# Optimization experiments

Measured on AMD Instinct MI355X. Metric: run time of the kernel, lower is better.

## Reference

```python
import jax, jax.numpy as jnp
import numpy as np

N = 50000        # nodes
E = 800000       # directed edges (before self-loops)
F_IN = 128       # num_features
GAT_DIM = 16     # per-head channels
HEADS = 4
HID = GAT_DIM * HEADS   # 64, concat output of each GATConv
FC = 10 * GAT_DIM       # 160
OUT = 64                # output_dim
NEG_SLOPE = 0.2         # PyG GATConv default


def _gat_conv(x, W, a_src, a_dst, b, src, dst):
    """One PyG-style GATConv (concat=True, self-loops already in src/dst).
    x: [N, Fin], W: [Fin, HEADS*GAT_DIM], a_src/a_dst: [HEADS, GAT_DIM], b: [HEADS*GAT_DIM]."""
    H, C = a_src.shape
    h = (x @ W).reshape(N, H, C)                       # [N,H,C]
    s_src = (h * a_src).sum(-1)                        # [N,H] per-node src score
    s_dst = (h * a_dst).sum(-1)                        # [N,H]
    e = jax.nn.leaky_relu(s_src[src] + s_dst[dst], NEG_SLOPE)  # [Etot,H]
    # segment softmax over incoming edges of each destination node
    m = jax.ops.segment_max(e, dst, num_segments=N)    # [N,H]
    ex = jnp.exp(e - m[dst])
    z = jax.ops.segment_sum(ex, dst, num_segments=N)   # [N,H]
    alpha = ex / (z[dst] + 1e-16)                      # [Etot,H]
    msg = h[src] * alpha[:, :, None]                   # [Etot,H,C]
    out = jax.ops.segment_sum(msg, dst, num_segments=N)
    return out.reshape(N, H * C) + b


def setup_inputs() -> dict:
    key = jax.random.key(0)
    ks = jax.random.split(key, 20)
    sc = 0.05
    inp = {
        "x": jax.random.normal(ks[0], (N, F_IN), dtype=jnp.float32),
        "edge_index": jax.random.randint(ks[1], (2, E), 0, N, dtype=jnp.int32),
        "W0": jax.random.normal(ks[2], (F_IN, HID), dtype=jnp.float32) * sc,
        "as0": jax.random.normal(ks[3], (HEADS, GAT_DIM), dtype=jnp.float32) * sc,
        "ad0": jax.random.normal(ks[4], (HEADS, GAT_DIM), dtype=jnp.float32) * sc,
        "b0": jnp.zeros((HID,), jnp.float32),
        "W1": jax.random.normal(ks[5], (HID, HID), dtype=jnp.float32) * sc,
        "as1": jax.random.normal(ks[6], (HEADS, GAT_DIM), dtype=jnp.float32) * sc,
        "ad1": jax.random.normal(ks[7], (HEADS, GAT_DIM), dtype=jnp.float32) * sc,
        "b1": jnp.zeros((HID,), jnp.float32),
        "W2": jax.random.normal(ks[8], (HID, HID), dtype=jnp.float32) * sc,
        "as2": jax.random.normal(ks[9], (HEADS, GAT_DIM), dtype=jnp.float32) * sc,
        "ad2": jax.random.normal(ks[10], (HEADS, GAT_DIM), dtype=jnp.float32) * sc,
        "b2": jnp.zeros((HID,), jnp.float32),
        "fw1": jax.random.normal(ks[11], (HID, FC), dtype=jnp.float32) * sc,
        "fb1": jnp.zeros((FC,), jnp.float32),
        "fw2": jax.random.normal(ks[12], (FC, OUT), dtype=jnp.float32) * sc,
        "fb2": jnp.zeros((OUT,), jnp.float32),
    }
    return inp


def reference(x, edge_index, W0, as0, ad0, b0, W1, as1, ad1, b1, W2, as2, ad2, b2, fw1, fb1, fw2, fb2):
    loop = jnp.arange(N, dtype=edge_index.dtype)
    src = jnp.concatenate([edge_index[0], loop])   # PyG add_self_loops=True
    dst = jnp.concatenate([edge_index[1], loop])
    h = jax.nn.relu(_gat_conv(x, W0, as0, ad0, b0, src, dst))
    h = jax.nn.relu(_gat_conv(h, W1, as1, ad1, b1, src, dst))
    h = jax.nn.relu(_gat_conv(h, W2, as2, ad2, b2, src, dst))
    h = jax.nn.relu(h @ fw1 + fb1)
    return h @ fw2 + fb2
```

## Files before the change

### kernel.cpp

```cpp
#include <hip/hip_runtime.h>
#include <hip/hip_fp16.h>

#define NN 50000
#define EE 800000
#define ETOT (EE + NN)
#define HIDD 64
#define NHEADS 4
#define FCD 160
#define OUTD 64

#define NBKT 196
#define BSTRIDE 5120
#define CHUNK 4096
#define NEBLK ((ETOT + CHUNK - 1) / CHUNK)
#define NGB   ((NN + 63) / 64)
#define NFC128 ((NN + 127) / 128)


__global__ void k_zero(int* __restrict__ cursor) {
    int t = threadIdx.x;
    if (t < NBKT) cursor[t] = 0;
}

__global__ __launch_bounds__(256) void k_binwrite(const int* __restrict__ ei,
                                                  int* __restrict__ cursor,
                                                  unsigned* __restrict__ binned) {
    __shared__ int hist[NBKT];
    __shared__ int sbase[NBKT];
    __shared__ int cur[NBKT];
    int t = threadIdx.x;
    for (int i = t; i < NBKT; i += 256) hist[i] = 0;
    __syncthreads();
    int base = blockIdx.x * CHUNK;
    for (int k = t; k < CHUNK; k += 256) {
        int i = base + k;
        if (i < ETOT) {
            int dst = (i < EE) ? ei[EE + i] : (i - EE);
            atomicAdd(&hist[dst >> 8], 1);
        }
    }
    __syncthreads();
    for (int b = t; b < NBKT; b += 256) {
        int c = hist[b];
        sbase[b] = b * BSTRIDE + (c ? atomicAdd(&cursor[b], c) : 0);
        cur[b] = 0;
    }
    __syncthreads();
    for (int k = t; k < CHUNK; k += 256) {
        int i = base + k;
        if (i < ETOT) {
            int src, dst;
            if (i < EE) { src = ei[i]; dst = ei[EE + i]; }
            else { src = dst = i - EE; }
            int b = dst >> 8;
            int p = atomicAdd(&cur[b], 1);
            binned[sbase[b] + p] = ((unsigned)src << 8) | (unsigned)(dst & 255);
        }
    }
}

__global__ __launch_bounds__(256) void k_csr_final(const int* __restrict__ cursor,
                                                   const unsigned* __restrict__ binned,
                                                   int* __restrict__ rowbeg,
                                                   int* __restrict__ rowend,
                                                   int* __restrict__ csrc) {
    __shared__ int hist[256];
    __shared__ int cur[256];
    __shared__ int wsum[4];
    int b = blockIdx.x;
    int t = threadIdx.x;
    int s0 = b * BSTRIDE;
    int cnt = cursor[b];
    hist[t] = 0;
    __syncthreads();
    for (int k = t; k < cnt; k += 256) {
        unsigned pr = binned[s0 + k];
        atomicAdd(&hist[pr & 255u], 1);
    }
    __syncthreads();
    int v = hist[t];
    int lane = t & 63, w = t >> 6;
    int x = v;
    #pragma unroll
    for (int off = 1; off < 64; off <<= 1) {
        int y = __shfl_up(x, off);
        if (lane >= off) x += y;
    }
    if (lane == 63) wsum[w] = x;
    __syncthreads();
    int add = 0;
    #pragma unroll
    for (int k = 0; k < 4; k++) add += (k < w) ? wsum[k] : 0;
    int excl = x + add - v;
    int n = (b << 8) + t;
    if (n < NN) {
        rowbeg[n] = s0 + excl;
        rowend[n] = s0 + excl + v;
    }
    cur[t] = s0 + excl;
    __syncthreads();
    for (int k = t; k < cnt; k += 256) {
        unsigned pr = binned[s0 + k];
        int p = atomicAdd(&cur[pr & 255u], 1);
        csrc[p] = (int)(pr >> 8);
    }
}


template<int FIN>
__global__ __launch_bounds__(256) void k_gemm_scores(
        const float* __restrict__ x, const float* __restrict__ W,
        const float* __restrict__ a_src, const float* __restrict__ a_dst,
        __half* __restrict__ h, float* __restrict__ ssrc, float* __restrict__ sdst) {
    __shared__ float wl[64 * 64];
    __shared__ float xt[64][68];
    int t = threadIdx.x;
    int nb = blockIdx.x * 64;
    int qg = t & 15, ng = t >> 4;
    float acc[4][4] = {};
    const float4* wl4 = (const float4*)wl;

    #pragma unroll
    for (int p = 0; p < FIN / 64; p++) {
        if (p) __syncthreads();
        for (int i = t; i < 64 * 64 / 4; i += 256)
            ((float4*)wl)[i] = ((const float4*)W)[p * 1024 + i];
        #pragma unroll
        for (int r = 0; r < 4; r++) {
            int idx = t + r * 256;
            int node = idx & 63, kq = idx >> 6;
            int n = nb + node;
            float4 v = make_float4(0.f, 0.f, 0.f, 0.f);
            if (n < NN) v = *(const float4*)(x + (size_t)n * FIN + p * 64 + kq * 4);
            xt[kq * 4 + 0][node] = v.x;
            xt[kq * 4 + 1][node] = v.y;
            xt[kq * 4 + 2][node] = v.z;
            xt[kq * 4 + 3][node] = v.w;
        }
        __syncthreads();
        #pragma unroll 4
        for (int k = 0; k < 64; k++) {
            float4 wv = wl4[k * 16 + qg];
            float4 xv = *(const float4*)&xt[k][ng * 4];
            acc[0][0] += xv.x * wv.x; acc[0][1] += xv.x * wv.y;
            acc[0][2] += xv.x * wv.z; acc[0][3] += xv.x * wv.w;
            acc[1][0] += xv.y * wv.x; acc[1][1] += xv.y * wv.y;
            acc[1][2] += xv.y * wv.z; acc[1][3] += xv.y * wv.w;
            acc[2][0] += xv.z * wv.x; acc[2][1] += xv.z * wv.y;
            acc[2][2] += xv.z * wv.z; acc[2][3] += xv.z * wv.w;
            acc[3][0] += xv.w * wv.x; acc[3][1] += xv.w * wv.y;
            acc[3][2] += xv.w * wv.z; acc[3][3] += xv.w * wv.w;
        }
    }

    #pragma unroll
    for (int r = 0; r < 4; r++) {
        int n = nb + ng * 4 + r;
        if (n < NN) {
            union { __half2 h2[2]; uint2 u; } pk;
            pk.h2[0] = __floats2half2_rn(acc[r][0], acc[r][1]);
            pk.h2[1] = __floats2half2_rn(acc[r][2], acc[r][3]);
            *(uint2*)(h + (size_t)n * HIDD + qg * 4) = pk.u;
        }
    }

    float as0 = a_src[qg * 4 + 0], as1 = a_src[qg * 4 + 1];
    float as2 = a_src[qg * 4 + 2], as3 = a_src[qg * 4 + 3];
    float ad0 = a_dst[qg * 4 + 0], ad1 = a_dst[qg * 4 + 1];
    float ad2 = a_dst[qg * 4 + 2], ad3 = a_dst[qg * 4 + 3];
    float vs[4], vd[4];
    #pragma unroll
    for (int r = 0; r < 4; r++) {
        vs[r] = acc[r][0] * as0 + acc[r][1] * as1 + acc[r][2] * as2 + acc[r][3] * as3;
        vd[r] = acc[r][0] * ad0 + acc[r][1] * ad1 + acc[r][2] * ad2 + acc[r][3] * ad3;
        vs[r] += __shfl_xor(vs[r], 1); vs[r] += __shfl_xor(vs[r], 2);
        vd[r] += __shfl_xor(vd[r], 1); vd[r] += __shfl_xor(vd[r], 2);
    }
    if ((qg & 3) == 0) {
        int hd = qg >> 2;
        #pragma unroll
        for (int r = 0; r < 4; r++) {
            int n = nb + ng * 4 + r;
            if (n < NN) {
                ssrc[n * NHEADS + hd] = vs[r];
                sdst[n * NHEADS + hd] = vd[r];
            }
        }
    }
}


__global__ __launch_bounds__(256) void k_aggr(
        const __half* __restrict__ h, const float* __restrict__ ssrc,
        const float* __restrict__ sdst, const int* __restrict__ rowbeg,
        const int* __restrict__ rowend,
        const int* __restrict__ csrc, const float* __restrict__ bias,
        float* __restrict__ out) {
    int wid  = threadIdx.x >> 6;
    int lane = threadIdx.x & 63;
    int n = blockIdx.x * 4 + wid;
    int sub = lane >> 4;
    int c4  = lane & 15;
    int hd  = c4 >> 2;
    int beg = rowbeg[n], end = rowend[n];
    float sdh = sdst[n * NHEADS + hd];

    float4 acc = make_float4(0.f, 0.f, 0.f, 0.f);
    float z = 0.f;
    for (int cb = beg; cb < end; cb += 16) {
        #pragma unroll
        for (int o = 0; o < 4; o++) {
            int e = cb + sub + o * 4;
            if (e < end) {
                int s = csrc[e];
                float eh = ssrc[s * NHEADS + hd] + sdh;
                eh = eh > 0.f ? eh : 0.2f * eh;
                float w = __expf(eh);
                uint2 r = *(const uint2*)(h + (size_t)s * HIDD + c4 * 4);
                float2 lo = __half22float2(*(__half2*)&r.x);
                float2 hi = __half22float2(*(__half2*)&r.y);
                acc.x += lo.x * w; acc.y += lo.y * w;
                acc.z += hi.x * w; acc.w += hi.y * w;
                z += w;
            }
        }
    }
    acc.x += __shfl_xor(acc.x, 16); acc.y += __shfl_xor(acc.y, 16);
    acc.z += __shfl_xor(acc.z, 16); acc.w += __shfl_xor(acc.w, 16);
    z += __shfl_xor(z, 16);
    acc.x += __shfl_xor(acc.x, 32); acc.y += __shfl_xor(acc.y, 32);
    acc.z += __shfl_xor(acc.z, 32); acc.w += __shfl_xor(acc.w, 32);
    z += __shfl_xor(z, 32);

    if (sub == 0) {
        float inv_z = 1.0f / (z + 1e-16f);
        float4 bv = *(const float4*)(bias + c4 * 4);
        float4 o;
        o.x = acc.x * inv_z + bv.x; o.x = o.x > 0.f ? o.x : 0.f;
        o.y = acc.y * inv_z + bv.y; o.y = o.y > 0.f ? o.y : 0.f;
        o.z = acc.z * inv_z + bv.z; o.z = o.z > 0.f ? o.z : 0.f;
        o.w = acc.w * inv_z + bv.w; o.w = o.w > 0.f ? o.w : 0.f;
        *(float4*)(out + (size_t)n * HIDD + c4 * 4) = o;
    }
}


__global__ __launch_bounds__(256) void k_fc_fused(const float* __restrict__ x,
        const float* __restrict__ W1, const float* __restrict__ b1,
        const float* __restrict__ W2, const float* __restrict__ b2,
        float* __restrict__ out) {
    __shared__ float wl[32 * 160];
    __shared__ float xt[32][132];
    __shared__ __half y[160][136];
    int t = threadIdx.x;
    int nb = blockIdx.x * 128;
    const float4* wl4 = (const float4*)wl;

    {
        int qg = t & 7, ng = t >> 3;
        float acc[4][5][4] = {};
        #pragma unroll
        for (int p = 0; p < 2; p++) {
            if (p) __syncthreads();
            for (int i = t; i < 32 * 160 / 4; i += 256)
                ((float4*)wl)[i] = ((const float4*)W1)[p * 32 * 40 + i];
            #pragma unroll
            for (int r = 0; r < 4; r++) {
                int idx = t + r * 256;
                int node = idx & 127, kq = idx >> 7;
                int n = nb + node;
                float4 v = make_float4(0.f, 0.f, 0.f, 0.f);
                if (n < NN) v = *(const float4*)(x + (size_t)n * 64 + p * 32 + kq * 4);
                xt[kq * 4 + 0][node] = v.x;
                xt[kq * 4 + 1][node] = v.y;
                xt[kq * 4 + 2][node] = v.z;
                xt[kq * 4 + 3][node] = v.w;
            }
            __syncthreads();
            #pragma unroll 4
            for (int k = 0; k < 32; k++) {
                float4 xv = *(const float4*)&xt[k][ng * 4];
                #pragma unroll
                for (int i = 0; i < 5; i++) {
                    float4 wv = wl4[k * 40 + qg + 8 * i];
                    acc[0][i][0] += xv.x * wv.x; acc[0][i][1] += xv.x * wv.y;
                    acc[0][i][2] += xv.x * wv.z; acc[0][i][3] += xv.x * wv.w;
                    acc[1][i][0] += xv.y * wv.x; acc[1][i][1] += xv.y * wv.y;
                    acc[1][i][2] += xv.y * wv.z; acc[1][i][3] += xv.y * wv.w;
                    acc[2][i][0] += xv.z * wv.x; acc[2][i][1] += xv.z * wv.y;
                    acc[2][i][2] += xv.z * wv.z; acc[2][i][3] += xv.z * wv.w;
                    acc[3][i][0] += xv.w * wv.x; acc[3][i][1] += xv.w * wv.y;
                    acc[3][i][2] += xv.w * wv.z; acc[3][i][3] += xv.w * wv.w;
                }
            }
        }
        #pragma unroll
        for (int i = 0; i < 5; i++) {
            int j0 = (qg + 8 * i) * 4;
            float4 bv = *(const float4*)(b1 + j0);
            #pragma unroll
            for (int r = 0; r < 4; r++) {
                int node = ng * 4 + r;
                float v0 = acc[r][i][0] + bv.x; v0 = v0 > 0.f ? v0 : 0.f;
                float v1 = acc[r][i][1] + bv.y; v1 = v1 > 0.f ? v1 : 0.f;
                float v2 = acc[r][i][2] + bv.z; v2 = v2 > 0.f ? v2 : 0.f;
                float v3 = acc[r][i][3] + bv.w; v3 = v3 > 0.f ? v3 : 0.f;
                y[j0 + 0][node] = __float2half_rn(v0);
                y[j0 + 1][node] = __float2half_rn(v1);
                y[j0 + 2][node] = __float2half_rn(v2);
                y[j0 + 3][node] = __float2half_rn(v3);
            }
        }
    }
    __syncthreads();

    {
        int qg = t & 15, ng = t >> 4;
        float acc[8][4] = {};
        #pragma unroll
        for (int p = 0; p < 2; p++) {
            if (p) __syncthreads();
            for (int i = t; i < 80 * 64 / 4; i += 256)
                ((float4*)wl)[i] = ((const float4*)W2)[p * 80 * 16 + i];
            __syncthreads();
            #pragma unroll 2
            for (int k = 0; k < 80; k++) {
                float4 wv = wl4[k * 16 + qg];
                uint4 yr = *(const uint4*)&y[p * 80 + k][ng * 8];
                float2 f0 = __half22float2(*(__half2*)&yr.x);
                float2 f1 = __half22float2(*(__half2*)&yr.y);
                float2 f2 = __half22float2(*(__half2*)&yr.z);
                float2 f3 = __half22float2(*(__half2*)&yr.w);
                acc[0][0] += f0.x * wv.x; acc[0][1] += f0.x * wv.y;
                acc[0][2] += f0.x * wv.z; acc[0][3] += f0.x * wv.w;
                acc[1][0] += f0.y * wv.x; acc[1][1] += f0.y * wv.y;
                acc[1][2] += f0.y * wv.z; acc[1][3] += f0.y * wv.w;
                acc[2][0] += f1.x * wv.x; acc[2][1] += f1.x * wv.y;
                acc[2][2] += f1.x * wv.z; acc[2][3] += f1.x * wv.w;
                acc[3][0] += f1.y * wv.x; acc[3][1] += f1.y * wv.y;
                acc[3][2] += f1.y * wv.z; acc[3][3] += f1.y * wv.w;
                acc[4][0] += f2.x * wv.x; acc[4][1] += f2.x * wv.y;
                acc[4][2] += f2.x * wv.z; acc[4][3] += f2.x * wv.w;
                acc[5][0] += f2.y * wv.x; acc[5][1] += f2.y * wv.y;
                acc[5][2] += f2.y * wv.z; acc[5][3] += f2.y * wv.w;
                acc[6][0] += f3.x * wv.x; acc[6][1] += f3.x * wv.y;
                acc[6][2] += f3.x * wv.z; acc[6][3] += f3.x * wv.w;
                acc[7][0] += f3.y * wv.x; acc[7][1] += f3.y * wv.y;
                acc[7][2] += f3.y * wv.z; acc[7][3] += f3.y * wv.w;
            }
        }
        int j0 = qg * 4;
        float4 bv = *(const float4*)(b2 + j0);
        #pragma unroll
        for (int r = 0; r < 8; r++) {
            int n = nb + ng * 8 + r;
            if (n < NN) {
                float4 o;
                o.x = acc[r][0] + bv.x; o.y = acc[r][1] + bv.y;
                o.z = acc[r][2] + bv.z; o.w = acc[r][3] + bv.w;
                *(float4*)(out + (size_t)n * 64 + j0) = o;
            }
        }
    }
}


extern "C" void kernel_launch(void* const* d_in, const int* in_sizes, int n_in,
                              void* d_out, int out_size, void* d_ws, size_t ws_size,
                              hipStream_t stream) {
    const float* x   = (const float*)d_in[0];
    const int*   ei  = (const int*)d_in[1];
    const float* W0  = (const float*)d_in[2];
    const float* as0 = (const float*)d_in[3];
    const float* ad0 = (const float*)d_in[4];
    const float* b0  = (const float*)d_in[5];
    const float* W1  = (const float*)d_in[6];
    const float* as1 = (const float*)d_in[7];
    const float* ad1 = (const float*)d_in[8];
    const float* b1  = (const float*)d_in[9];
    const float* W2  = (const float*)d_in[10];
    const float* as2 = (const float*)d_in[11];
    const float* ad2 = (const float*)d_in[12];
    const float* b2  = (const float*)d_in[13];
    const float* fw1 = (const float*)d_in[14];
    const float* fb1 = (const float*)d_in[15];
    const float* fw2 = (const float*)d_in[16];
    const float* fb2 = (const float*)d_in[17];

    float* ws     = (float*)d_ws;
    __half* h_buf = (__half*)ws;
    float* ssrc   = ws + (size_t)NN * HIDD;
    float* sdst   = ssrc + (size_t)NN * NHEADS;
    float* act    = sdst + (size_t)NN * NHEADS;
    float* fcb    = act + (size_t)NN * HIDD;
    unsigned* binned = (unsigned*)fcb;
    int*   csrc   = (int*)fcb + 2000000;
    int*   rowbeg = (int*)fcb + 4000000;
    int*   rowend = (int*)fcb + 4100000;
    int*   cursor = (int*)(fcb + (size_t)NN * FCD);

    k_zero<<<1, 256, 0, stream>>>(cursor);
    k_binwrite<<<NEBLK, 256, 0, stream>>>(ei, cursor, binned);
    k_csr_final<<<NBKT, 256, 0, stream>>>(cursor, binned, rowbeg, rowend, csrc);

    k_gemm_scores<128><<<NGB, 256, 0, stream>>>(x, W0, as0, ad0, h_buf, ssrc, sdst);
    k_aggr<<<NN / 4, 256, 0, stream>>>(h_buf, ssrc, sdst, rowbeg, rowend, csrc, b0, act);
    k_gemm_scores<64><<<NGB, 256, 0, stream>>>(act, W1, as1, ad1, h_buf, ssrc, sdst);
    k_aggr<<<NN / 4, 256, 0, stream>>>(h_buf, ssrc, sdst, rowbeg, rowend, csrc, b1, act);
    k_gemm_scores<64><<<NGB, 256, 0, stream>>>(act, W2, as2, ad2, h_buf, ssrc, sdst);
    k_aggr<<<NN / 4, 256, 0, stream>>>(h_buf, ssrc, sdst, rowbeg, rowend, csrc, b2, act);

    k_fc_fused<<<NFC128, 256, 0, stream>>>(act, fw1, fb1, fw2, fb2, (float*)d_out);
}
```

Measured before the change: 233.9 us.

## Fuse GAT aggregation with next layer's GEMM and score computation

Adds a kernel that aggregates 64 destination nodes per block, applies bias and ReLU, keeps the activations in shared memory, and immediately multiplies by the next layer's weight to produce fp16 h and attention scores. This removes the fp32 activation round trip through global memory and two kernel launches for layers 1 and 2, with ping-pong buffers for h and scores. In exchange the aggregation now runs 8 nodes sequentially per wavefront in larger 512-thread blocks with about 33KB of shared memory, which may lower occupancy and the latency hiding of the gathers. The softmax drops the max subtraction, as the existing aggregation appears to do.

```diff
diff --git a/kernel.cpp b/kernel.cpp
--- a/kernel.cpp
+++ b/kernel.cpp
@@ -184,6 +184,126 @@
             if (n < NN) {
                 ssrc[n * NHEADS + hd] = vs[r];
                 sdst[n * NHEADS + hd] = vd[r];
+            }
+        }
+    }
+}
+
+
+__global__ __launch_bounds__(512) void k_aggr_gemm(
+        const __half* __restrict__ h, const float* __restrict__ ssrc,
+        const float* __restrict__ sdst, const int* __restrict__ rowbeg,
+        const int* __restrict__ rowend, const int* __restrict__ csrc,
+        const float* __restrict__ bias, const float* __restrict__ W,
+        const float* __restrict__ a_src, const float* __restrict__ a_dst,
+        __half* __restrict__ hout, float* __restrict__ ssrc_o,
+        float* __restrict__ sdst_o) {
+    __shared__ float wl[64 * 64];
+    __shared__ float xt[64][68];
+    int t = threadIdx.x;
+    int nb = blockIdx.x * 64;
+
+    for (int i = t; i < 64 * 64 / 4; i += 512)
+        ((float4*)wl)[i] = ((const float4*)W)[i];
+
+    {
+        int wid = t >> 6, lane = t & 63;
+        int sub = lane >> 4, c4 = lane & 15, hd = c4 >> 2;
+        #pragma unroll 1
+        for (int i = 0; i < 8; i++) {
+            int nl = wid * 8 + i;
+            int n = nb + nl;
+            float4 acc = make_float4(0.f, 0.f, 0.f, 0.f);
+            float z = 0.f;
+            if (n < NN) {
+                int beg = rowbeg[n], end = rowend[n];
+                float sdh = sdst[n * NHEADS + hd];
+                for (int cb = beg; cb < end; cb += 16) {
+                    #pragma unroll
+                    for (int o = 0; o < 4; o++) {
+                        int e = cb + sub + o * 4;
+                        if (e < end) {
+                            int s = csrc[e];
+                            float eh = ssrc[s * NHEADS + hd] + sdh;
+                            eh = eh > 0.f ? eh : 0.2f * eh;
+                            float w = __expf(eh);
+                            uint2 r = *(const uint2*)(h + (size_t)s * HIDD + c4 * 4);
+                            float2 lo = __half22float2(*(__half2*)&r.x);
+                            float2 hi = __half22float2(*(__half2*)&r.y);
+                            acc.x += lo.x * w; acc.y += lo.y * w;
+                            acc.z += hi.x * w; acc.w += hi.y * w;
+                            z += w;
+                        }
+                    }
+                }
+            }
+            acc.x += __shfl_xor(acc.x, 16); acc.y += __shfl_xor(acc.y, 16);
+            acc.z += __shfl_xor(acc.z, 16); acc.w += __shfl_xor(acc.w, 16);
+            z += __shfl_xor(z, 16);
+            acc.x += __shfl_xor(acc.x, 32); acc.y += __shfl_xor(acc.y, 32);
+            acc.z += __shfl_xor(acc.z, 32); acc.w += __shfl_xor(acc.w, 32);
+            z += __shfl_xor(z, 32);
+            if (sub == 0) {
+                float inv_z = 1.0f / (z + 1e-16f);
+                float4 bv = *(const float4*)(bias + c4 * 4);
+                float v0 = acc.x * inv_z + bv.x; v0 = v0 > 0.f ? v0 : 0.f;
+                float v1 = acc.y * inv_z + bv.y; v1 = v1 > 0.f ? v1 : 0.f;
+                float v2 = acc.z * inv_z + bv.z; v2 = v2 > 0.f ? v2 : 0.f;
+                float v3 = acc.w * inv_z + bv.w; v3 = v3 > 0.f ? v3 : 0.f;
+                if (n >= NN) { v0 = v1 = v2 = v3 = 0.f; }
+                xt[c4 * 4 + 0][nl] = v0;
+                xt[c4 * 4 + 1][nl] = v1;
+                xt[c4 * 4 + 2][nl] = v2;
+                xt[c4 * 4 + 3][nl] = v3;
+            }
+        }
+    }
+    __syncthreads();
+
+    {
+        int qg = t & 15, ng = t >> 4;
+        float acc[2][4] = {};
+        const float4* wl4 = (const float4*)wl;
+        #pragma unroll 4
+        for (int k = 0; k < 64; k++) {
+            float4 wv = wl4[k * 16 + qg];
+            float2 xv = *(const float2*)&xt[k][ng * 2];
+            acc[0][0] += xv.x * wv.x; acc[0][1] += xv.x * wv.y;
+            acc[0][2] += xv.x * wv.z; acc[0][3] += xv.x * wv.w;
+            acc[1][0] += xv.y * wv.x; acc[1][1] += xv.y * wv.y;
+            acc[1][2] += xv.y * wv.z; acc[1][3] += xv.y * wv.w;
+        }
+        #pragma unroll
+        for (int r = 0; r < 2; r++) {
+            int n = nb + ng * 2 + r;
+            if (n < NN) {
+                union { __half2 h2[2]; uint2 u; } pk;
+                pk.h2[0] = __floats2half2_rn(acc[r][0], acc[r][1]);
+                pk.h2[1] = __floats2half2_rn(acc[r][2], acc[r][3]);
+                *(uint2*)(hout + (size_t)n * HIDD + qg * 4) = pk.u;
+            }
+        }
+        float as0 = a_src[qg * 4 + 0], as1 = a_src[qg * 4 + 1];
+        float as2 = a_src[qg * 4 + 2], as3 = a_src[qg * 4 + 3];
+        float ad0 = a_dst[qg * 4 + 0], ad1 = a_dst[qg * 4 + 1];
+        float ad2 = a_dst[qg * 4 + 2], ad3 = a_dst[qg * 4 + 3];
+        float vs[2], vd[2];
+        #pragma unroll
+        for (int r = 0; r < 2; r++) {
+            vs[r] = acc[r][0] * as0 + acc[r][1] * as1 + acc[r][2] * as2 + acc[r][3] * as3;
+            vd[r] = acc[r][0] * ad0 + acc[r][1] * ad1 + acc[r][2] * ad2 + acc[r][3] * ad3;
+            vs[r] += __shfl_xor(vs[r], 1); vs[r] += __shfl_xor(vs[r], 2);
+            vd[r] += __shfl_xor(vd[r], 1); vd[r] += __shfl_xor(vd[r], 2);
+        }
+        if ((qg & 3) == 0) {
+            int hd = qg >> 2;
+            #pragma unroll
+            for (int r = 0; r < 2; r++) {
+                int n = nb + ng * 2 + r;
+                if (n < NN) {
+                    ssrc_o[n * NHEADS + hd] = vs[r];
+                    sdst_o[n * NHEADS + hd] = vd[r];
+                }
             }
         }
     }
@@ -387,28 +507,31 @@
     const float* fw2 = (const float*)d_in[16];
     const float* fb2 = (const float*)d_in[17];
 
-    float* ws     = (float*)d_ws;
-    __half* h_buf = (__half*)ws;
-    float* ssrc   = ws + (size_t)NN * HIDD;
-    float* sdst   = ssrc + (size_t)NN * NHEADS;
-    float* act    = sdst + (size_t)NN * NHEADS;
-    float* fcb    = act + (size_t)NN * HIDD;
-    unsigned* binned = (unsigned*)fcb;
-    int*   csrc   = (int*)fcb + 2000000;
-    int*   rowbeg = (int*)fcb + 4000000;
-    int*   rowend = (int*)fcb + 4100000;
-    int*   cursor = (int*)(fcb + (size_t)NN * FCD);
+    float* ws = (float*)d_ws;
+    __half* hA  = (__half*)ws;
+    __half* hB  = (__half*)(ws + (size_t)NN * 32);
+    float* sAsrc = ws + (size_t)NN * 64;
+    float* sAdst = sAsrc + (size_t)NN * NHEADS;
+    float* sBsrc = sAdst + (size_t)NN * NHEADS;
+    float* sBdst = sBsrc + (size_t)NN * NHEADS;
+    float* act   = sBdst + (size_t)NN * NHEADS;
+    float* scr   = act + (size_t)NN * HIDD;
+    unsigned* binned = (unsigned*)scr;
+    int*   csrc   = (int*)scr + 1100000;
+    int*   rowbeg = (int*)scr + 2200000;
+    int*   rowend = (int*)scr + 2300000;
+    int*   cursor = (int*)scr + 2400000;
 
     k_zero<<<1, 256, 0, stream>>>(cursor);
     k_binwrite<<<NEBLK, 256, 0, stream>>>(ei, cursor, binned);
     k_csr_final<<<NBKT, 256, 0, stream>>>(cursor, binned, rowbeg, rowend, csrc);
 
-    k_gemm_scores<128><<<NGB, 256, 0, stream>>>(x, W0, as0, ad0, h_buf, ssrc, sdst);
-    k_aggr<<<NN / 4, 256, 0, stream>>>(h_buf, ssrc, sdst, rowbeg, rowend, csrc, b0, act);
-    k_gemm_scores<64><<<NGB, 256, 0, stream>>>(act, W1, as1, ad1, h_buf, ssrc, sdst);
-    k_aggr<<<NN / 4, 256, 0, stream>>>(h_buf, ssrc, sdst, rowbeg, rowend, csrc, b1, act);
-    k_gemm_scores<64><<<NGB, 256, 0, stream>>>(act, W2, as2, ad2, h_buf, ssrc, sdst);
-    k_aggr<<<NN / 4, 256, 0, stream>>>(h_buf, ssrc, sdst, rowbeg, rowend, csrc, b2, act);
+    k_gemm_scores<128><<<NGB, 256, 0, stream>>>(x, W0, as0, ad0, hA, sAsrc, sAdst);
+    k_aggr_gemm<<<NGB, 512, 0, stream>>>(hA, sAsrc, sAdst, rowbeg, rowend, csrc,
+                                         b0, W1, as1, ad1, hB, sBsrc, sBdst);
+    k_aggr_gemm<<<NGB, 512, 0, stream>>>(hB, sBsrc, sBdst, rowbeg, rowend, csrc,
+                                         b1, W2, as2, ad2, hA, sAsrc, sAdst);
+    k_aggr<<<NN / 4, 256, 0, stream>>>(hA, sAsrc, sAdst, rowbeg, rowend, csrc, b2, act);
 
     k_fc_fused<<<NFC128, 256, 0, stream>>>(act, fw1, fb1, fw2, fb2, (float*)d_out);
 }
```

Measured after the change: 222.3 us. -5.0%, faster.
